# Kernel optimization log

Hardware: AMD Instinct MI355X
Metric: run time of the kernel (lower is better)

The kernel has to match this reference:

```python
import jax, jax.numpy as jnp
import numpy as np

N, E, C, D, H = 50000, 1600000, 50000, 128, 512


def setup_inputs() -> dict:
    key = jax.random.key(0)
    ks = jax.random.split(key, 16)
    s = jnp.float32(0.02)  # keep activations stable through 3 layers
    inp = {}
    inp["x"] = jax.random.normal(ks[0], (N, D), jnp.float32)
    inp["edge_index"] = jax.random.randint(ks[1], (2, E), 0, N)
    inp["first_edge"] = jax.random.randint(ks[2], (2,), 0, N)
    inp["candidate_edges"] = jax.random.randint(ks[3], (C, 2), 0, N)
    inp["t"] = jax.random.uniform(ks[4], (1, 1), jnp.float32)
    dims = [(D, H), (H, H), (H, H)]
    i = 5
    for l, (di, do) in enumerate(dims):
        inp[f"gin{l}_w1"] = jax.random.normal(ks[i], (di, do), jnp.float32) * s; i += 1
        inp[f"gin{l}_b1"] = jnp.zeros((do,), jnp.float32)
        inp[f"gin{l}_w2"] = jax.random.normal(ks[i], (do, do), jnp.float32) * s; i += 1
        inp[f"gin{l}_b2"] = jnp.zeros((do,), jnp.float32)
    inp["pred_w1"] = jax.random.normal(ks[i], (5 * H, H), jnp.float32) * s; i += 1
    inp["pred_b1"] = jnp.zeros((H,), jnp.float32)
    inp["pred_w2"] = jax.random.normal(ks[i], (H, 1), jnp.float32) * s; i += 1
    inp["pred_b2"] = jnp.zeros((1,), jnp.float32)
    inp["time_w1"] = jax.random.normal(ks[i], (1, H), jnp.float32) * s; i += 1
    inp["time_b1"] = jnp.zeros((H,), jnp.float32)
    inp["time_w2"] = jax.random.normal(ks[i], (H, H), jnp.float32) * s; i += 1
    inp["time_b2"] = jnp.zeros((H,), jnp.float32)
    return inp


def _edge_rep(x, u, v):
    # 'sum_absdiff': cat([x_u + x_v, |x_u - x_v|]) -> 2*H features
    xu, xv = x[u], x[v]
    return jnp.concatenate([xu + xv, jnp.abs(xu - xv)], axis=-1)


def reference(x, edge_index, first_edge, candidate_edges, t,
              gin0_w1, gin0_b1, gin0_w2, gin0_b2,
              gin1_w1, gin1_b1, gin1_w2, gin1_b2,
              gin2_w1, gin2_b1, gin2_w2, gin2_b2,
              pred_w1, pred_b1, pred_w2, pred_b2,
              time_w1, time_b1, time_w2, time_b2):
    src, dst = edge_index[0], edge_index[1]
    layers = [(gin0_w1, gin0_b1, gin0_w2, gin0_b2),
              (gin1_w1, gin1_b1, gin1_w2, gin1_b2),
              (gin2_w1, gin2_b1, gin2_w2, gin2_b2)]
    # GINConv (eps=0): h_i = MLP(x_i + sum_{j->i} x_j)
    for w1, b1, w2, b2 in layers:
        agg = jax.ops.segment_sum(x[src], dst, num_segments=x.shape[0])
        h = x + agg
        x = jax.nn.relu(h @ w1 + b1) @ w2 + b2
    first_feat = _edge_rep(x, first_edge[0], first_edge[1])  # [2H]
    t_embed = (jax.nn.relu(t @ time_w1 + time_b1) @ time_w2 + time_b2)[0]  # [H]
    cand_feat = _edge_rep(x, candidate_edges[:, 0], candidate_edges[:, 1])  # [C, 2H]
    Cn = cand_feat.shape[0]
    feat = jnp.concatenate([
        jnp.broadcast_to(first_feat, (Cn, first_feat.shape[0])),
        cand_feat,
        jnp.broadcast_to(t_embed, (Cn, t_embed.shape[0])),
    ], axis=-1)  # [C, 5H]
    logits = (jax.nn.relu(feat @ pred_w1 + pred_b1) @ pred_w2 + pred_b2)[:, 0]  # [C]
    return logits
```

## Files before the change

### kernel.cpp

```cpp
#include <hip/hip_runtime.h>

typedef __bf16 bf16x2 __attribute__((ext_vector_type(2)));
typedef __bf16 bf16x4 __attribute__((ext_vector_type(4)));
typedef __bf16 bf16x8 __attribute__((ext_vector_type(8)));
typedef float f32x4 __attribute__((ext_vector_type(4)));

#define CSR_CHUNKS 256

__global__ __launch_bounds__(256)
void hist_part_kernel(const int* __restrict__ dst, int* __restrict__ deg, int E, int N) {
    const int r = blockIdx.x & 7;
    const int chunk = blockIdx.x >> 3;
    const int RS = (N + 7) >> 3;
    const int lo = r * RS;
    const int hi = min(lo + RS, N);
    const int stride = CSR_CHUNKS * 256;
    for (int i = chunk * 256 + threadIdx.x; i < E; i += stride) {
        int d = dst[i];
        if (d >= lo && d < hi) atomicAdd(&deg[d], 1);
    }
}

__global__ __launch_bounds__(256)
void scatter_part_kernel(const int* __restrict__ src, const int* __restrict__ dst,
                         int* __restrict__ cursor, int* __restrict__ colsrc, int E, int N) {
    const int r = blockIdx.x & 7;
    const int chunk = blockIdx.x >> 3;
    const int RS = (N + 7) >> 3;
    const int lo = r * RS;
    const int hi = min(lo + RS, N);
    const int stride = CSR_CHUNKS * 256;
    for (int i = chunk * 256 + threadIdx.x; i < E; i += stride) {
        int d = dst[i];
        if (d >= lo && d < hi) {
            int p = atomicAdd(&cursor[d], 1);
            colsrc[p] = src[i];
        }
    }
}

__global__ __launch_bounds__(256)
void blocksum_kernel(const int* __restrict__ deg, int* __restrict__ bsum, int n) {
    __shared__ int red[256];
    int i = blockIdx.x * 256 + threadIdx.x;
    red[threadIdx.x] = (i < n) ? deg[i] : 0;
    __syncthreads();
    for (int off = 128; off > 0; off >>= 1) {
        if (threadIdx.x < off) red[threadIdx.x] += red[threadIdx.x + off];
        __syncthreads();
    }
    if (threadIdx.x == 0) bsum[blockIdx.x] = red[0];
}

__global__ __launch_bounds__(256)
void scanb_kernel(int* __restrict__ bsum, int nb) {
    __shared__ int s[256];
    int t = threadIdx.x;
    s[t] = (t < nb) ? bsum[t] : 0;
    __syncthreads();
    for (int off = 1; off < 256; off <<= 1) {
        int v = (t >= off) ? s[t - off] : 0;
        __syncthreads();
        s[t] += v;
        __syncthreads();
    }
    if (t < nb) bsum[t] = (t == 0) ? 0 : s[t - 1];
}

__global__ __launch_bounds__(256)
void scanw_kernel(const int* __restrict__ deg, const int* __restrict__ bsum,
                  int* __restrict__ rowptr, int* __restrict__ cursor, int n) {
    __shared__ int s[256];
    int b = blockIdx.x, t = threadIdx.x;
    int i = b * 256 + t;
    int d = (i < n) ? deg[i] : 0;
    s[t] = d;
    __syncthreads();
    for (int off = 1; off < 256; off <<= 1) {
        int v = (t >= off) ? s[t - off] : 0;
        __syncthreads();
        s[t] += v;
        __syncthreads();
    }
    int incl = s[t];
    int base = bsum[b];
    if (i < n) {
        int r = base + incl - d;
        rowptr[i] = r;
        cursor[i] = r;
        if (i == n - 1) rowptr[n] = base + incl;
    }
}

__global__ void f32_to_bf16_kernel(const float* __restrict__ in, __bf16* __restrict__ out, int n4) {
    int i = blockIdx.x * 256 + threadIdx.x;
    if (i < n4) {
        float4 f = ((const float4*)in)[i];
        bf16x4 o;
        o[0] = (__bf16)f.x; o[1] = (__bf16)f.y; o[2] = (__bf16)f.z; o[3] = (__bf16)f.w;
        ((bf16x4*)out)[i] = o;
    }
}

__global__ void wprep_kernel(const float* __restrict__ in, __bf16* __restrict__ out, int kbits) {
    int idx = blockIdx.x * 256 + threadIdx.x;
    int K = 1 << kbits;
    if (idx < (512 << kbits)) {
        int k = idx & (K - 1);
        int n = idx >> kbits;
        out[idx] = (__bf16)in[k * 512 + n];
    }
}

template<int F> struct VecT;
template<> struct VecT<2> { using T = bf16x2; };
template<> struct VecT<4> { using T = bf16x4; };
template<> struct VecT<8> { using T = bf16x8; };

template<int F, int U, int STR>
__global__ __launch_bounds__(256)
void agg_kernel(const __bf16* __restrict__ xb, const int* __restrict__ rowptr,
                const int* __restrict__ colsrc, __bf16* __restrict__ h, int n, int colbase) {
    const int node = blockIdx.x * 4 + (threadIdx.x >> 6);
    if (node >= n) return;
    const int lane = threadIdx.x & 63;
    using V = typename VecT<F>::T;

    const __bf16* xl = xb + colbase + lane * F;

    float acc[F];
    {
        V v = *(const V*)(xl + (size_t)node * STR);
        #pragma unroll
        for (int i = 0; i < F; i++) acc[i] = (float)v[i];
    }

    int e   = __builtin_amdgcn_readfirstlane(rowptr[node]);
    int end = __builtin_amdgcn_readfirstlane(rowptr[node + 1]);

    for (; e + U <= end; e += U) {
        int s[U];
        #pragma unroll
        for (int j = 0; j < U; j++) s[j] = colsrc[e + j];
        V v[U];
        #pragma unroll
        for (int j = 0; j < U; j++) v[j] = *(const V*)(xl + (size_t)s[j] * STR);
        #pragma unroll
        for (int j = 0; j < U; j++)
            #pragma unroll
            for (int i = 0; i < F; i++) acc[i] += (float)v[j][i];
    }
    if constexpr (U > 4) {
        for (; e + 4 <= end; e += 4) {
            int s[4];
            #pragma unroll
            for (int j = 0; j < 4; j++) s[j] = colsrc[e + j];
            V v[4];
            #pragma unroll
            for (int j = 0; j < 4; j++) v[j] = *(const V*)(xl + (size_t)s[j] * STR);
            #pragma unroll
            for (int j = 0; j < 4; j++)
                #pragma unroll
                for (int i = 0; i < F; i++) acc[i] += (float)v[j][i];
        }
    }
    for (; e < end; e++) {
        int s0 = colsrc[e];
        V v = *(const V*)(xl + (size_t)s0 * STR);
        #pragma unroll
        for (int i = 0; i < F; i++) acc[i] += (float)v[i];
    }

    __bf16* out = h + colbase + (size_t)node * STR + lane * F;
    V o;
    #pragma unroll
    for (int i = 0; i < F; i++) o[i] = (__bf16)acc[i];
    *(V*)out = o;
}

template<int AMODE, bool RELU>
__global__ __launch_bounds__(256, 3)
void gemm_kernel(const __bf16* __restrict__ A, const __bf16* __restrict__ Xb,
                 const int* __restrict__ cand, const __bf16* __restrict__ Bt,
                 const float* __restrict__ bias, __bf16* __restrict__ Cout,
                 int M, int K) {
    __shared__ __bf16 smem[2 * (2048 + 8192)];
    __bf16* const sA0 = smem;
    __bf16* const sA1 = smem + 2048;
    __bf16* const sB0 = smem + 4096;
    __bf16* const sB1 = smem + 4096 + 8192;

    const int tid = threadIdx.x;
    const int lane = tid & 63;
    const int wid = tid >> 6;
    const int mlane = lane & 15;
    const int quad = lane >> 4;
    const int rowBase = blockIdx.x * 64;
    const int nBase = blockIdx.y * 256;

    const int ar = tid >> 2;
    const int acn = tid & 3;
    const int ac = acn << 3;

    const int wkey = (ar >> 1) & 3;
    const int woffA = ar * 32 + ((acn ^ wkey) << 3);
    const int rkey = (mlane >> 1) & 3;
    const int base_r = mlane * 32 + ((quad ^ rkey) << 3);

    const f32x4 fzero = {0.f, 0.f, 0.f, 0.f};
    f32x4 acc[4][4];
    #pragma unroll
    for (int i = 0; i < 4; i++)
        #pragma unroll
        for (int j = 0; j < 4; j++) acc[i][j] = fzero;

    int uu = 0, vv = 0;
    const int grow = rowBase + ar;
    const bool arowok = (grow < M);
    if (AMODE == 1 && arowok) { uu = cand[2 * grow]; vv = cand[2 * grow + 1]; }

    struct PF { bf16x8 pa, pxu, pxv; bf16x8 pb[4]; int pk; };
    PF s0, s1;

    auto issue = [&](PF& S, int k0) {
        S.pk = k0;
        if (AMODE == 0) {
            S.pa = bf16x8{};
            if (arowok) S.pa = *(const bf16x8*)(A + (size_t)grow * K + k0 + ac);
        } else {
            if (arowok) {
                int kk = (k0 + ac) & 511;
                S.pxu = *(const bf16x8*)(Xb + (size_t)uu * 512 + kk);
                S.pxv = *(const bf16x8*)(Xb + (size_t)vv * 512 + kk);
            }
        }
        #pragma unroll
        for (int c = 0; c < 4; c++)
            S.pb[c] = *(const bf16x8*)(Bt + (size_t)(nBase + ar + c * 64) * K + k0 + ac);
    };

    auto commit = [&](PF& S, __bf16* bufA, __bf16* bufB) {
        bf16x8 av;
        if (AMODE == 0) {
            av = S.pa;
        } else {
            av = bf16x8{};
            if (arowok) {
                if (S.pk + ac < 512) {
                    #pragma unroll
                    for (int q = 0; q < 8; q++) av[q] = (__bf16)((float)S.pxu[q] + (float)S.pxv[q]);
                } else {
                    #pragma unroll
                    for (int q = 0; q < 8; q++) av[q] = (__bf16)fabsf((float)S.pxu[q] - (float)S.pxv[q]);
                }
            }
        }
        *(bf16x8*)(bufA + woffA) = av;
        #pragma unroll
        for (int c = 0; c < 4; c++)
            *(bf16x8*)(bufB + woffA + c * 2048) = S.pb[c];
    };

    auto compute = [&](const __bf16* bufA, const __bf16* bufB) {
        bf16x8 aF[4], bF[4];
        #pragma unroll
        for (int mt = 0; mt < 4; mt++)
            aF[mt] = *(const bf16x8*)(bufA + mt * 512 + base_r);
        #pragma unroll
        for (int nt = 0; nt < 4; nt++)
            bF[nt] = *(const bf16x8*)(bufB + wid * 2048 + nt * 512 + base_r);
        #pragma unroll
        for (int mt = 0; mt < 4; mt++)
            #pragma unroll
            for (int nt = 0; nt < 4; nt++)
                acc[mt][nt] = __builtin_amdgcn_mfma_f32_16x16x32_bf16(aF[mt], bF[nt], acc[mt][nt], 0, 0, 0);
    };

    issue(s0, 0);
    commit(s0, sA0, sB0);
    issue(s1, 32);
    __syncthreads();

    for (int k0 = 0; k0 < K; k0 += 64) {
        if (k0 + 64 < K) issue(s0, k0 + 64);
        compute(sA0, sB0);
        commit(s1, sA1, sB1);
        __syncthreads();
        if (k0 + 96 < K) issue(s1, k0 + 96);
        compute(sA1, sB1);
        if (k0 + 64 < K) commit(s0, sA0, sB0);
        __syncthreads();
    }

    float bv[4];
    #pragma unroll
    for (int nt = 0; nt < 4; nt++) bv[nt] = bias[nBase + wid * 64 + nt * 16 + mlane];

    float* tp = (float*)smem;
    const int erow = tid >> 4;
    const int ecg = tid & 15;
    #pragma unroll
    for (int mt = 0; mt < 4; mt++) {
        __syncthreads();
        #pragma unroll
        for (int nt = 0; nt < 4; nt++) {
            #pragma unroll
            for (int r = 0; r < 4; r++) {
                float v = acc[mt][nt][r] + bv[nt];
                if (RELU) v = fmaxf(v, 0.f);
                tp[(quad * 4 + r) * 260 + wid * 64 + nt * 16 + mlane] = v;
            }
        }
        __syncthreads();
        int gr = rowBase + mt * 16 + erow;
        if (gr < M) {
            const float* rp = tp + erow * 260 + ecg * 16;
            f32x4 a = *(const f32x4*)(rp);
            f32x4 b = *(const f32x4*)(rp + 4);
            f32x4 c = *(const f32x4*)(rp + 8);
            f32x4 d = *(const f32x4*)(rp + 12);
            bf16x8 o0, o1;
            #pragma unroll
            for (int j = 0; j < 4; j++) { o0[j] = (__bf16)a[j]; o0[4 + j] = (__bf16)b[j]; }
            #pragma unroll
            for (int j = 0; j < 4; j++) { o1[j] = (__bf16)c[j]; o1[4 + j] = (__bf16)d[j]; }
            __bf16* op = Cout + (size_t)gr * 512 + nBase + ecg * 16;
            *(bf16x8*)op = o0;
            *(bf16x8*)(op + 8) = o1;
        }
    }
}

__global__ __launch_bounds__(512)
void constvec_kernel(const __bf16* __restrict__ xb, const int* __restrict__ first_edge,
                     const float* __restrict__ t,
                     const float* __restrict__ tw1, const float* __restrict__ tb1,
                     const float* __restrict__ tw2, const float* __restrict__ tb2,
                     const float* __restrict__ pw1, const float* __restrict__ pb1,
                     float* __restrict__ cvec) {
    __shared__ float z1[512];
    __shared__ float te[512];
    __shared__ float ff[1024];
    int tid = threadIdx.x;
    float tv = t[0];
    z1[tid] = fmaxf(tv * tw1[tid] + tb1[tid], 0.f);
    int u = first_edge[0], v = first_edge[1];
    float xu = (float)xb[(size_t)u * 512 + tid];
    float xv = (float)xb[(size_t)v * 512 + tid];
    ff[tid] = xu + xv;
    ff[512 + tid] = fabsf(xu - xv);
    __syncthreads();
    float s = tb2[tid];
    for (int j = 0; j < 512; j++) s += z1[j] * tw2[j * 512 + tid];
    te[tid] = s;
    __syncthreads();
    float c = pb1[tid];
    for (int k = 0; k < 1024; k++) c += ff[k] * pw1[k * 512 + tid];
    for (int j = 0; j < 512; j++) c += te[j] * pw1[(2048 + j) * 512 + tid];
    cvec[tid] = c;
}

__global__ __launch_bounds__(256)
void logits_kernel(const __bf16* __restrict__ Z, const float* __restrict__ w2,
                   const float* __restrict__ b2, float* __restrict__ out, int C) {
    int c = blockIdx.x * 4 + (threadIdx.x >> 6);
    if (c >= C) return;
    int lane = threadIdx.x & 63;
    bf16x8 z = *(const bf16x8*)(Z + (size_t)c * 512 + lane * 8);
    const float4* w = (const float4*)(w2 + lane * 8);
    float4 w0 = w[0], w1 = w[1];
    float s = (float)z[0] * w0.x + (float)z[1] * w0.y + (float)z[2] * w0.z + (float)z[3] * w0.w
            + (float)z[4] * w1.x + (float)z[5] * w1.y + (float)z[6] * w1.z + (float)z[7] * w1.w;
    #pragma unroll
    for (int off = 32; off > 0; off >>= 1) s += __shfl_down(s, off);
    if (lane == 0) out[c] = s + b2[0];
}

extern "C" void kernel_launch(void* const* d_in, const int* in_sizes, int n_in,
                              void* d_out, int out_size, void* d_ws, size_t ws_size,
                              hipStream_t stream) {
    (void)n_in; (void)out_size; (void)ws_size;
    const float* x          = (const float*)d_in[0];
    const int*   edge_index = (const int*)d_in[1];
    const int*   first_edge = (const int*)d_in[2];
    const int*   cand       = (const int*)d_in[3];
    const float* t          = (const float*)d_in[4];
    const float* gw1[3] = {(const float*)d_in[5], (const float*)d_in[9],  (const float*)d_in[13]};
    const float* gb1[3] = {(const float*)d_in[6], (const float*)d_in[10], (const float*)d_in[14]};
    const float* gw2[3] = {(const float*)d_in[7], (const float*)d_in[11], (const float*)d_in[15]};
    const float* gb2[3] = {(const float*)d_in[8], (const float*)d_in[12], (const float*)d_in[16]};
    const float* pw1 = (const float*)d_in[17];
    const float* pb1 = (const float*)d_in[18];
    const float* pw2 = (const float*)d_in[19];
    const float* pb2 = (const float*)d_in[20];
    const float* tw1 = (const float*)d_in[21];
    const float* tb1 = (const float*)d_in[22];
    const float* tw2 = (const float*)d_in[23];
    const float* tb2 = (const float*)d_in[24];

    const int N = in_sizes[0] / 128;
    const int E = in_sizes[1] / 2;
    const int C = in_sizes[3] / 2;

    char* p = (char*)d_ws;
    auto alloc = [&](size_t bytes) -> void* {
        void* r = (void*)p;
        p += (bytes + 255) & ~(size_t)255;
        return r;
    };
    __bf16* h    = (__bf16*)alloc((size_t)N * 512 * 2);
    __bf16* u    = (__bf16*)alloc((size_t)N * 512 * 2);
    __bf16* xb   = (__bf16*)alloc((size_t)N * 512 * 2);
    __bf16* wt01 = (__bf16*)alloc((size_t)512 * 128 * 2);
    __bf16* wt02 = (__bf16*)alloc((size_t)512 * 512 * 2);
    __bf16* wt11 = (__bf16*)alloc((size_t)512 * 512 * 2);
    __bf16* wt12 = (__bf16*)alloc((size_t)512 * 512 * 2);
    __bf16* wt21 = (__bf16*)alloc((size_t)512 * 512 * 2);
    __bf16* wt22 = (__bf16*)alloc((size_t)512 * 512 * 2);
    __bf16* wtH  = (__bf16*)alloc((size_t)512 * 1024 * 2);
    int* rowptr = (int*)alloc((size_t)(N + 1) * 4);
    int* deg    = (int*)alloc((size_t)N * 4);
    int* cursor = (int*)alloc((size_t)N * 4);
    int* colsrc = (int*)alloc((size_t)E * 4);
    int* bsum   = (int*)alloc((size_t)256 * 4);
    float* cvec = (float*)alloc(512 * 4);
    __bf16* xb0 = (__bf16*)u;

    const int* src = edge_index;
    const int* dst = edge_index + E;

    hipMemsetAsync(deg, 0, (size_t)N * 4, stream);
    int nb = (N + 255) / 256;
    hist_part_kernel<<<CSR_CHUNKS * 8, 256, 0, stream>>>(dst, deg, E, N);
    blocksum_kernel<<<nb, 256, 0, stream>>>(deg, bsum, N);
    scanb_kernel<<<1, 256, 0, stream>>>(bsum, nb);
    scanw_kernel<<<nb, 256, 0, stream>>>(deg, bsum, rowptr, cursor, N);
    scatter_part_kernel<<<CSR_CHUNKS * 8, 256, 0, stream>>>(src, dst, cursor, colsrc, E, N);

    f32_to_bf16_kernel<<<((N * 128 / 4) + 255) / 256, 256, 0, stream>>>(x, xb0, N * 128 / 4);
    wprep_kernel<<<((512 << 7)  + 255) / 256, 256, 0, stream>>>(gw1[0], wt01, 7);
    wprep_kernel<<<((512 << 9)  + 255) / 256, 256, 0, stream>>>(gw2[0], wt02, 9);
    wprep_kernel<<<((512 << 9)  + 255) / 256, 256, 0, stream>>>(gw1[1], wt11, 9);
    wprep_kernel<<<((512 << 9)  + 255) / 256, 256, 0, stream>>>(gw2[1], wt12, 9);
    wprep_kernel<<<((512 << 9)  + 255) / 256, 256, 0, stream>>>(gw1[2], wt21, 9);
    wprep_kernel<<<((512 << 9)  + 255) / 256, 256, 0, stream>>>(gw2[2], wt22, 9);
    wprep_kernel<<<((512 << 10) + 255) / 256, 256, 0, stream>>>(pw1 + (size_t)1024 * 512, wtH, 10);

    dim3 ggrid((N + 63) / 64, 2);
    int ablocks = (N + 3) / 4;

    agg_kernel<2, 16, 128><<<ablocks, 256, 0, stream>>>(xb0, rowptr, colsrc, h, N, 0);
    gemm_kernel<0, true ><<<ggrid, 256, 0, stream>>>(h, nullptr, nullptr, wt01, gb1[0], u,  N, 128);
    gemm_kernel<0, false><<<ggrid, 256, 0, stream>>>(u, nullptr, nullptr, wt02, gb2[0], xb, N, 512);
    agg_kernel<4, 8, 512><<<ablocks, 256, 0, stream>>>(xb, rowptr, colsrc, h, N, 0);
    agg_kernel<4, 8, 512><<<ablocks, 256, 0, stream>>>(xb, rowptr, colsrc, h, N, 256);
    gemm_kernel<0, true ><<<ggrid, 256, 0, stream>>>(h, nullptr, nullptr, wt11, gb1[1], u,  N, 512);
    gemm_kernel<0, false><<<ggrid, 256, 0, stream>>>(u, nullptr, nullptr, wt12, gb2[1], xb, N, 512);
    agg_kernel<4, 8, 512><<<ablocks, 256, 0, stream>>>(xb, rowptr, colsrc, h, N, 0);
    agg_kernel<4, 8, 512><<<ablocks, 256, 0, stream>>>(xb, rowptr, colsrc, h, N, 256);
    gemm_kernel<0, true ><<<ggrid, 256, 0, stream>>>(h, nullptr, nullptr, wt21, gb1[2], u,  N, 512);
    gemm_kernel<0, false><<<ggrid, 256, 0, stream>>>(u, nullptr, nullptr, wt22, gb2[2], xb, N, 512);

    constvec_kernel<<<1, 512, 0, stream>>>(xb, first_edge, t, tw1, tb1, tw2, tb2, pw1, pb1, cvec);
    dim3 hgrid((C + 63) / 64, 2);
    gemm_kernel<1, true><<<hgrid, 256, 0, stream>>>(nullptr, xb, cand, wtH, cvec, u, C, 1024);
    logits_kernel<<<(C + 3) / 4, 256, 0, stream>>>(u, pw2, pb2, (float*)d_out, C);
}
```

Baseline: 1.210 ms.

## Stage GEMM A/B tiles with direct global-to-LDS loads

Replaces the register-staged prefetch of the weight (B) tile and the dense A tile with global_load_lds instructions that write straight into shared memory with a matching XOR swizzle. The gathered candidate-edge A path still goes through registers. The aim is to cut VGPR pressure and the extra LDS store instructions per K-step, freeing registers and issue slots for the MFMA loop. The risk is that the async LDS writes and the swizzle layout have to line up with the barriers and the reader indexing, and rows past M are left unwritten in the A buffer.

```diff
diff --git a/kernel.cpp b/kernel.cpp
--- a/kernel.cpp
+++ b/kernel.cpp
@@ -6,6 +6,11 @@
 typedef float f32x4 __attribute__((ext_vector_type(4)));
 
 #define CSR_CHUNKS 256
+
+__device__ __forceinline__ void gload16(const __bf16* g, __bf16* l) {
+    __builtin_amdgcn_global_load_lds((const __attribute__((address_space(1))) void*)g,
+                                     (__attribute__((address_space(3))) void*)l, 16, 0, 0);
+}
 
 __global__ __launch_bounds__(256)
 void hist_part_kernel(const int* __restrict__ dst, int* __restrict__ deg, int E, int N) {
@@ -198,14 +203,21 @@
     const int rowBase = blockIdx.x * 64;
     const int nBase = blockIdx.y * 256;
 
+    const int swzc = (((lane & 3) ^ ((lane >> 3) & 3)) << 3);
+
+    const int aRow = rowBase + wid * 16 + (lane >> 2);
+    const __bf16* aSrc = A + (size_t)aRow * K + swzc;
+    const int bRow = nBase + wid * 64 + (lane >> 2);
+    const __bf16* bSrc = Bt + (size_t)bRow * K + swzc;
+
+    const int rkey = (mlane >> 1) & 3;
+    const int base_r = mlane * 32 + ((quad ^ rkey) << 3);
+
     const int ar = tid >> 2;
     const int acn = tid & 3;
     const int ac = acn << 3;
-
     const int wkey = (ar >> 1) & 3;
     const int woffA = ar * 32 + ((acn ^ wkey) << 3);
-    const int rkey = (mlane >> 1) & 3;
-    const int base_r = mlane * 32 + ((quad ^ rkey) << 3);
 
     const f32x4 fzero = {0.f, 0.f, 0.f, 0.f};
     f32x4 acc[4][4];
@@ -219,46 +231,37 @@
     const bool arowok = (grow < M);
     if (AMODE == 1 && arowok) { uu = cand[2 * grow]; vv = cand[2 * grow + 1]; }
 
-    struct PF { bf16x8 pa, pxu, pxv; bf16x8 pb[4]; int pk; };
-    PF s0, s1;
-
-    auto issue = [&](PF& S, int k0) {
-        S.pk = k0;
-        if (AMODE == 0) {
-            S.pa = bf16x8{};
-            if (arowok) S.pa = *(const bf16x8*)(A + (size_t)grow * K + k0 + ac);
-        } else {
-            if (arowok) {
-                int kk = (k0 + ac) & 511;
-                S.pxu = *(const bf16x8*)(Xb + (size_t)uu * 512 + kk);
-                S.pxv = *(const bf16x8*)(Xb + (size_t)vv * 512 + kk);
+    bf16x8 pxu{}, pxv{};
+    int pk = 0;
+
+    auto stageB = [&](__bf16* bufB, int k0) {
+        #pragma unroll
+        for (int j = 0; j < 4; j++)
+            gload16(bSrc + (size_t)j * 16 * K + k0, bufB + wid * 2048 + j * 512);
+    };
+    auto stageA0 = [&](__bf16* bufA, int k0) {
+        if (aRow < M) gload16(aSrc + k0, bufA + wid * 512);
+    };
+    auto issueA1 = [&](int k0) {
+        pk = k0;
+        if (arowok) {
+            int kk = (k0 + ac) & 511;
+            pxu = *(const bf16x8*)(Xb + (size_t)uu * 512 + kk);
+            pxv = *(const bf16x8*)(Xb + (size_t)vv * 512 + kk);
+        }
+    };
+    auto commitA1 = [&](__bf16* bufA) {
+        bf16x8 av = bf16x8{};
+        if (arowok) {
+            if (pk + ac < 512) {
+                #pragma unroll
+                for (int q = 0; q < 8; q++) av[q] = (__bf16)((float)pxu[q] + (float)pxv[q]);
+            } else {
+                #pragma unroll
+                for (int q = 0; q < 8; q++) av[q] = (__bf16)fabsf((float)pxu[q] - (float)pxv[q]);
             }
         }
-        #pragma unroll
-        for (int c = 0; c < 4; c++)
-            S.pb[c] = *(const bf16x8*)(Bt + (size_t)(nBase + ar + c * 64) * K + k0 + ac);
-    };
-
-    auto commit = [&](PF& S, __bf16* bufA, __bf16* bufB) {
-        bf16x8 av;
-        if (AMODE == 0) {
-            av = S.pa;
-        } else {
-            av = bf16x8{};
-            if (arowok) {
-                if (S.pk + ac < 512) {
-                    #pragma unroll
-                    for (int q = 0; q < 8; q++) av[q] = (__bf16)((float)S.pxu[q] + (float)S.pxv[q]);
-                } else {
-                    #pragma unroll
-                    for (int q = 0; q < 8; q++) av[q] = (__bf16)fabsf((float)S.pxu[q] - (float)S.pxv[q]);
-                }
-            }
-        }
         *(bf16x8*)(bufA + woffA) = av;
-        #pragma unroll
-        for (int c = 0; c < 4; c++)
-            *(bf16x8*)(bufB + woffA + c * 2048) = S.pb[c];
     };
 
     auto compute = [&](const __bf16* bufA, const __bf16* bufB) {
@@ -276,25 +279,47 @@
                 acc[mt][nt] = __builtin_amdgcn_mfma_f32_16x16x32_bf16(aF[mt], bF[nt], acc[mt][nt], 0, 0, 0);
     };
 
-    issue(s0, 0);
-    commit(s0, sA0, sB0);
-    issue(s1, 32);
-    __syncthreads();
-
-    for (int k0 = 0; k0 < K; k0 += 64) {
-        if (k0 + 64 < K) issue(s0, k0 + 64);
-        compute(sA0, sB0);
-        commit(s1, sA1, sB1);
-        __syncthreads();
-        if (k0 + 96 < K) issue(s1, k0 + 96);
-        compute(sA1, sB1);
-        if (k0 + 64 < K) commit(s0, sA0, sB0);
-        __syncthreads();
+    const int nt = K >> 5;
+    if (AMODE == 0) {
+        stageA0(sA0, 0);
+        stageB(sB0, 0);
+        __syncthreads();
+        for (int t = 0; t < nt; t += 2) {
+            stageA0(sA1, (t + 1) << 5);
+            stageB(sB1, (t + 1) << 5);
+            compute(sA0, sB0);
+            __syncthreads();
+            if (t + 2 < nt) {
+                stageA0(sA0, (t + 2) << 5);
+                stageB(sB0, (t + 2) << 5);
+            }
+            compute(sA1, sB1);
+            __syncthreads();
+        }
+    } else {
+        issueA1(0);
+        commitA1(sA0);
+        stageB(sB0, 0);
+        __syncthreads();
+        for (int t = 0; t < nt; t += 2) {
+            issueA1((t + 1) << 5);
+            stageB(sB1, (t + 1) << 5);
+            compute(sA0, sB0);
+            commitA1(sA1);
+            __syncthreads();
+            if (t + 2 < nt) {
+                issueA1((t + 2) << 5);
+                stageB(sB0, (t + 2) << 5);
+            }
+            compute(sA1, sB1);
+            if (t + 2 < nt) commitA1(sA0);
+            __syncthreads();
+        }
     }
 
     float bv[4];
     #pragma unroll
-    for (int nt = 0; nt < 4; nt++) bv[nt] = bias[nBase + wid * 64 + nt * 16 + mlane];
+    for (int nt2 = 0; nt2 < 4; nt2++) bv[nt2] = bias[nBase + wid * 64 + nt2 * 16 + mlane];
 
     float* tp = (float*)smem;
     const int erow = tid >> 4;
@@ -303,12 +328,12 @@
     for (int mt = 0; mt < 4; mt++) {
         __syncthreads();
         #pragma unroll
-        for (int nt = 0; nt < 4; nt++) {
+        for (int nt2 = 0; nt2 < 4; nt2++) {
             #pragma unroll
             for (int r = 0; r < 4; r++) {
-                float v = acc[mt][nt][r] + bv[nt];
+                float v = acc[mt][nt2][r] + bv[nt2];
                 if (RELU) v = fmaxf(v, 0.f);
-                tp[(quad * 4 + r) * 260 + wid * 64 + nt * 16 + mlane] = v;
+                tp[(quad * 4 + r) * 260 + wid * 64 + nt2 * 16 + mlane] = v;
             }
         }
         __syncthreads();
```

After: 1.202 ms. No clear change (-0.7%).
